# Optimization experiments

Measured on AMD Instinct MI355X. Metric: run time of the kernel, lower is better.

The kernel has to match this reference:

```python
import jax, jax.numpy as jnp
import numpy as np

E, N, H, F = 8, 16384, 1024, 4096  # experts, total tokens, hidden, ffn hidden

def setup_inputs() -> dict:
    key = jax.random.key(0)
    k1, k2, k3 = jax.random.split(key, 3)
    x = jax.random.normal(k1, (N, H), dtype=jnp.float32)
    # original uses torch.rand for weights -> uniform [0,1)
    w1 = jax.random.uniform(k2, (E, H, F), dtype=jnp.float32)
    w2 = jax.random.uniform(k3, (E, F, H), dtype=jnp.float32)
    tokens_per_expert = jnp.full((E,), N // E, dtype=jnp.int32)
    return {
        "permuted_local_hidden_states": x,
        "weight1": w1,
        "weight2": w2,
        "tokens_per_expert": tokens_per_expert,
    }

def reference(permuted_local_hidden_states, weight1, weight2, tokens_per_expert):
    # Grouped GEMM 1: per-expert x[rows_e] @ w1[e]  -> [N, F]
    fc1_output = jax.lax.ragged_dot(permuted_local_hidden_states, weight1, tokens_per_expert)
    # Unfused activation (F.gelu default = exact erf gelu)
    intermediate = jax.nn.gelu(fc1_output, approximate=False)
    # Grouped GEMM 2: per-expert act[rows_e] @ w2[e] -> [N, H]
    fc2_output = jax.lax.ragged_dot(intermediate, weight2, tokens_per_expert)
    return fc2_output
```

## Files before the change

### kernel.cpp

```cpp
#include <hip/hip_runtime.h>
#include <hip/hip_bf16.h>

typedef unsigned short u16;
typedef __attribute__((ext_vector_type(8))) __bf16 bf16x8;
typedef __attribute__((ext_vector_type(4))) float f32x4;
typedef __attribute__((ext_vector_type(4))) float f4v;
typedef __attribute__((ext_vector_type(2))) unsigned short u16x2;
typedef __attribute__((ext_vector_type(4))) unsigned short u16x4;
typedef __attribute__((ext_vector_type(8))) unsigned short u16x8;

__device__ __forceinline__ u16 f32_to_bf16(float f) {
  unsigned int u = __builtin_bit_cast(unsigned int, f);
  u += 0x7FFFu + ((u >> 16) & 1u);
  return (u16)(u >> 16);
}

__device__ __forceinline__ float fast_gelu(float v) {
  float v2 = v * v;
  float t = v * fmaf(0.0713548162726f, v2, 1.5957691216057308f);
  float e = __expf(-t);
  float s = __builtin_amdgcn_rcpf(1.0f + e);
  return v * s;
}

__device__ __forceinline__ void async_ld16(const void* gsrc, void* ldst) {
  __builtin_amdgcn_global_load_lds(
      (__attribute__((address_space(1))) void*)(unsigned long long)gsrc,
      (__attribute__((address_space(3))) void*)(unsigned long long)ldst,
      16, 0, 0);
}

__global__ void cvt_kernel(const float* __restrict__ in, u16* __restrict__ out, int n8) {
  int i = blockIdx.x * blockDim.x + threadIdx.x;
  if (i >= n8) return;
  const f4v* p = (const f4v*)(in + (size_t)i * 8);
  f4v a = p[0], b = p[1];
  u16x8 r;
  r[0] = f32_to_bf16(a[0]); r[1] = f32_to_bf16(a[1]);
  r[2] = f32_to_bf16(a[2]); r[3] = f32_to_bf16(a[3]);
  r[4] = f32_to_bf16(b[0]); r[5] = f32_to_bf16(b[1]);
  r[6] = f32_to_bf16(b[2]); r[7] = f32_to_bf16(b[3]);
  *(u16x8*)(out + (size_t)i * 8) = r;
}

__global__ __launch_bounds__(256)
void tpose_cvt_kernel(const float* __restrict__ in, u16* __restrict__ out, int R, int C) {
  __shared__ u16 tile[64 * 66];
  const int e = blockIdx.z;
  const int c0 = blockIdx.x * 64, r0 = blockIdx.y * 64;
  const float* src = in + (size_t)e * R * C;
  u16* dst = out + (size_t)e * R * C;
  const int t = threadIdx.x;
#pragma unroll
  for (int i = 0; i < 4; ++i) {
    int idx = i * 256 + t;
    int row = idx >> 4, c4 = idx & 15;
    f4v v = *(const f4v*)&src[(size_t)(r0 + row) * C + (c0 + c4 * 4)];
    u16x2 lo, hi;
    lo[0] = f32_to_bf16(v[0]); lo[1] = f32_to_bf16(v[1]);
    hi[0] = f32_to_bf16(v[2]); hi[1] = f32_to_bf16(v[3]);
    *(u16x2*)&tile[row * 66 + c4 * 4] = lo;
    *(u16x2*)&tile[row * 66 + c4 * 4 + 2] = hi;
  }
  __syncthreads();
#pragma unroll
  for (int i = 0; i < 4; ++i) {
    int idx = i * 256 + t;
    int c = idx >> 4, r4 = idx & 15;
    u16x4 v;
#pragma unroll
    for (int j = 0; j < 4; ++j) v[j] = tile[(r4 * 4 + j) * 66 + c];
    *(u16x4*)&dst[(size_t)(c0 + c) * R + r0 + r4 * 4] = v;
  }
}

template <int FUSE>
__global__ __launch_bounds__(512, 2)
void grouped_gemm(const u16* __restrict__ A, const u16* __restrict__ Bt,
                  void* __restrict__ Out, const int* __restrict__ tokens,
                  int Mtot, int K, int Nn) {
  const int NT = Nn >> 8;
  const int id = blockIdx.x;
  const int xcd = id & 7;
  const int within = id >> 3;
  const int slot = xcd + 8 * (within / NT);
  const int ntile = within % NT;

  int row_start = 0, tiles_before = 0;
  int expert = -1, my_row0 = 0, rows_valid = 0;
#pragma unroll
  for (int e = 0; e < 8; ++e) {
    int tk = tokens[e];
    int nt = (tk + 255) >> 8;
    if (expert < 0 && slot >= tiles_before && slot < tiles_before + nt) {
      expert = e;
      int mi = slot - tiles_before;
      my_row0 = row_start + mi * 256;
      rows_valid = tk - mi * 256;
      if (rows_valid > 256) rows_valid = 256;
    }
    tiles_before += nt;
    row_start += tk;
  }
  if (expert < 0) return;

  const int n0 = ntile * 256;
  const u16* Bq = Bt + (size_t)expert * Nn * K + (size_t)n0 * K;

  __shared__ __align__(16) u16 lA[4][8192];
  __shared__ __align__(16) u16 lB[4][8192];

  const int tid = threadIdx.x;
  const int lane = tid & 63;
  const int wave = tid >> 6;
  const int wm = (wave >> 2) * 128;
  const int wn = (wave & 3) * 64;
  const int fr = lane & 15;
  const int fq = lane >> 4;

  f32x4 acc[8][4];
#pragma unroll
  for (int i = 0; i < 8; ++i)
#pragma unroll
    for (int j = 0; j < 4; ++j) acc[i][j] = (f32x4){0.f, 0.f, 0.f, 0.f};

  const int sr = tid >> 2;
  const int swz = ((tid & 3) ^ ((sr >> 1) & 3)) * 8;
  int ga0 = my_row0 + sr;        if (ga0 > Mtot - 1) ga0 = Mtot - 1;
  int ga1 = my_row0 + 128 + sr;  if (ga1 > Mtot - 1) ga1 = Mtot - 1;
  const u16* pA0 = A + (size_t)ga0 * K + swz;
  const u16* pA1 = A + (size_t)ga1 * K + swz;
  const u16* pB0 = Bq + (size_t)sr * K + swz;
  const u16* pB1 = Bq + (size_t)(128 + sr) * K + swz;

  const int cswz = (fq ^ ((fr >> 1) & 3)) * 8;
  const int aoff0 = (wm + fr) * 32 + cswz;
  const int boff0 = (wn + fr) * 32 + cswz;

  const int nslices = K >> 5;

#pragma unroll
  for (int s = 0; s < 3; ++s) {
    async_ld16(pA0 + s * 32, &lA[s][tid * 8]);
    async_ld16(pA1 + s * 32, &lA[s][4096 + tid * 8]);
    async_ld16(pB0 + s * 32, &lB[s][tid * 8]);
    async_ld16(pB1 + s * 32, &lB[s][4096 + tid * 8]);
  }

  bf16x8 aF[4], bF[4];
  for (int sl = 0; sl < nslices; ++sl) {
    const int b = sl & 3;
    const int nb = (sl + 3) & 3;
    const int sk = (sl + 3 < nslices ? sl + 3 : sl) * 32;

    asm volatile("s_waitcnt vmcnt(8)" ::: "memory");
    __builtin_amdgcn_s_barrier();
    asm volatile("" ::: "memory");

    async_ld16(pA0 + sk, &lA[nb][tid * 8]);
    async_ld16(pA1 + sk, &lA[nb][4096 + tid * 8]);
#pragma unroll
    for (int n = 0; n < 4; ++n) bF[n] = *(const bf16x8*)&lB[b][boff0 + n * 512];
#pragma unroll
    for (int m = 0; m < 4; ++m) aF[m] = *(const bf16x8*)&lA[b][aoff0 + m * 512];
    __builtin_amdgcn_s_setprio(1);
#pragma unroll
    for (int m = 0; m < 4; ++m)
#pragma unroll
      for (int n = 0; n < 4; ++n)
        acc[m][n] = __builtin_amdgcn_mfma_f32_16x16x32_bf16(aF[m], bF[n], acc[m][n], 0, 0, 0);
    __builtin_amdgcn_s_setprio(0);
    __builtin_amdgcn_s_barrier();
    asm volatile("" ::: "memory");

    async_ld16(pB0 + sk, &lB[nb][tid * 8]);
    async_ld16(pB1 + sk, &lB[nb][4096 + tid * 8]);
#pragma unroll
    for (int m = 0; m < 4; ++m) aF[m] = *(const bf16x8*)&lA[b][aoff0 + 2048 + m * 512];
    __builtin_amdgcn_s_setprio(1);
#pragma unroll
    for (int m = 0; m < 4; ++m)
#pragma unroll
      for (int n = 0; n < 4; ++n)
        acc[m + 4][n] = __builtin_amdgcn_mfma_f32_16x16x32_bf16(aF[m], bF[n], acc[m + 4][n], 0, 0, 0);
    __builtin_amdgcn_s_setprio(0);
  }

  if (FUSE) {
    u16* Op = (u16*)Out;
#pragma unroll
    for (int m = 0; m < 8; ++m) {
#pragma unroll
      for (int r = 0; r < 4; ++r) {
        int lrow = wm + m * 16 + fq * 4 + r;
        if (lrow < rows_valid) {
          size_t base = (size_t)(my_row0 + lrow) * Nn + (size_t)(n0 + wn + fr);
#pragma unroll
          for (int n = 0; n < 4; ++n)
            Op[base + n * 16] = f32_to_bf16(fast_gelu(acc[m][n][r]));
        }
      }
    }
  } else {
    float* Op = (float*)Out;
#pragma unroll
    for (int m = 0; m < 8; ++m) {
#pragma unroll
      for (int r = 0; r < 4; ++r) {
        int lrow = wm + m * 16 + fq * 4 + r;
        if (lrow < rows_valid) {
          size_t base = (size_t)(my_row0 + lrow) * Nn + (size_t)(n0 + wn + fr);
#pragma unroll
          for (int n = 0; n < 4; ++n) Op[base + n * 16] = acc[m][n][r];
        }
      }
    }
  }
}

extern "C" void kernel_launch(void* const* d_in, const int* in_sizes, int n_in,
                              void* d_out, int out_size, void* d_ws, size_t ws_size,
                              hipStream_t stream) {
  (void)in_sizes; (void)n_in; (void)out_size; (void)ws_size;
  const float* x  = (const float*)d_in[0];
  const float* w1 = (const float*)d_in[1];
  const float* w2 = (const float*)d_in[2];
  const int* tokens = (const int*)d_in[3];

  const int N = 16384, H = 1024, F = 4096, E = 8;

  u16* x_bf  = (u16*)d_ws;
  u16* w1t   = x_bf + (size_t)N * H;
  u16* w2t   = w1t + (size_t)E * F * H;
  u16* inter = w2t + (size_t)E * H * F;

  cvt_kernel<<<dim3((N * H / 8 + 255) / 256), dim3(256), 0, stream>>>(x, x_bf, N * H / 8);
  tpose_cvt_kernel<<<dim3(F / 64, H / 64, E), dim3(256), 0, stream>>>(w1, w1t, H, F);
  tpose_cvt_kernel<<<dim3(H / 64, F / 64, E), dim3(256), 0, stream>>>(w2, w2t, F, H);

  const int SLOTS = N / 256 + E;
  grouped_gemm<1><<<dim3((F / 256) * SLOTS), dim3(512), 0, stream>>>(
      x_bf, w1t, inter, tokens, N, H, F);
  grouped_gemm<0><<<dim3((H / 256) * SLOTS), dim3(512), 0, stream>>>(
      inter, w2t, (float*)d_out, tokens, N, F, H);
}
```

Before: 631.9 us.

## Use narrower N tile for second GEMM and single-barrier pipeline loop

Templates the grouped GEMM on its N tile width and launches the second GEMM with 128-wide tiles, doubling its grid so more CUs stay busy when the output is only 1024 wide. The main loop loads all fragments up front, issues every async load at once and drops the mid-iteration barrier. The transpose tile padding changes from 66 to 65 with scalar LDS writes to cut bank conflicts. Costs are lower B reuse per block in GEMM2, more register pressure from holding all A fragments, and a possible LDS write race now that the second barrier is gone.

```diff
diff --git a/kernel.cpp b/kernel.cpp
--- a/kernel.cpp
+++ b/kernel.cpp
@@ -5,7 +5,6 @@
 typedef __attribute__((ext_vector_type(8))) __bf16 bf16x8;
 typedef __attribute__((ext_vector_type(4))) float f32x4;
 typedef __attribute__((ext_vector_type(4))) float f4v;
-typedef __attribute__((ext_vector_type(2))) unsigned short u16x2;
 typedef __attribute__((ext_vector_type(4))) unsigned short u16x4;
 typedef __attribute__((ext_vector_type(8))) unsigned short u16x8;
 
@@ -45,7 +44,7 @@
 
 __global__ __launch_bounds__(256)
 void tpose_cvt_kernel(const float* __restrict__ in, u16* __restrict__ out, int R, int C) {
-  __shared__ u16 tile[64 * 66];
+  __shared__ u16 tile[64 * 65];
   const int e = blockIdx.z;
   const int c0 = blockIdx.x * 64, r0 = blockIdx.y * 64;
   const float* src = in + (size_t)e * R * C;
@@ -56,11 +55,11 @@
     int idx = i * 256 + t;
     int row = idx >> 4, c4 = idx & 15;
     f4v v = *(const f4v*)&src[(size_t)(r0 + row) * C + (c0 + c4 * 4)];
-    u16x2 lo, hi;
-    lo[0] = f32_to_bf16(v[0]); lo[1] = f32_to_bf16(v[1]);
-    hi[0] = f32_to_bf16(v[2]); hi[1] = f32_to_bf16(v[3]);
-    *(u16x2*)&tile[row * 66 + c4 * 4] = lo;
-    *(u16x2*)&tile[row * 66 + c4 * 4 + 2] = hi;
+    int base = row * 65 + c4 * 4;
+    tile[base + 0] = f32_to_bf16(v[0]);
+    tile[base + 1] = f32_to_bf16(v[1]);
+    tile[base + 2] = f32_to_bf16(v[2]);
+    tile[base + 3] = f32_to_bf16(v[3]);
   }
   __syncthreads();
 #pragma unroll
@@ -69,17 +68,20 @@
     int c = idx >> 4, r4 = idx & 15;
     u16x4 v;
 #pragma unroll
-    for (int j = 0; j < 4; ++j) v[j] = tile[(r4 * 4 + j) * 66 + c];
+    for (int j = 0; j < 4; ++j) v[j] = tile[(r4 * 4 + j) * 65 + c];
     *(u16x4*)&dst[(size_t)(c0 + c) * R + r0 + r4 * 4] = v;
   }
 }
 
-template <int FUSE>
+template <int FUSE, int BN>
 __global__ __launch_bounds__(512, 2)
 void grouped_gemm(const u16* __restrict__ A, const u16* __restrict__ Bt,
                   void* __restrict__ Out, const int* __restrict__ tokens,
                   int Mtot, int K, int Nn) {
-  const int NT = Nn >> 8;
+  constexpr int NF = BN / 64;
+  constexpr int BLOADS = BN / 128;
+  constexpr int LPS = 2 + BLOADS;
+  const int NT = Nn / BN;
   const int id = blockIdx.x;
   const int xcd = id & 7;
   const int within = id >> 3;
@@ -104,25 +106,25 @@
   }
   if (expert < 0) return;
 
-  const int n0 = ntile * 256;
+  const int n0 = ntile * BN;
   const u16* Bq = Bt + (size_t)expert * Nn * K + (size_t)n0 * K;
 
   __shared__ __align__(16) u16 lA[4][8192];
-  __shared__ __align__(16) u16 lB[4][8192];
+  __shared__ __align__(16) u16 lB[4][BN * 32];
 
   const int tid = threadIdx.x;
   const int lane = tid & 63;
   const int wave = tid >> 6;
   const int wm = (wave >> 2) * 128;
-  const int wn = (wave & 3) * 64;
+  const int wn = (wave & 3) * (BN / 4);
   const int fr = lane & 15;
   const int fq = lane >> 4;
 
-  f32x4 acc[8][4];
+  f32x4 acc[8][NF];
 #pragma unroll
   for (int i = 0; i < 8; ++i)
 #pragma unroll
-    for (int j = 0; j < 4; ++j) acc[i][j] = (f32x4){0.f, 0.f, 0.f, 0.f};
+    for (int j = 0; j < NF; ++j) acc[i][j] = (f32x4){0.f, 0.f, 0.f, 0.f};
 
   const int sr = tid >> 2;
   const int swz = ((tid & 3) ^ ((sr >> 1) & 3)) * 8;
@@ -131,7 +133,7 @@
   const u16* pA0 = A + (size_t)ga0 * K + swz;
   const u16* pA1 = A + (size_t)ga1 * K + swz;
   const u16* pB0 = Bq + (size_t)sr * K + swz;
-  const u16* pB1 = Bq + (size_t)(128 + sr) * K + swz;
+  const u16* pB1 = Bq + (size_t)((BN == 256 ? 128 : 0) + sr) * K + swz;
 
   const int cswz = (fq ^ ((fr >> 1) & 3)) * 8;
   const int aoff0 = (wm + fr) * 32 + cswz;
@@ -144,45 +146,43 @@
     async_ld16(pA0 + s * 32, &lA[s][tid * 8]);
     async_ld16(pA1 + s * 32, &lA[s][4096 + tid * 8]);
     async_ld16(pB0 + s * 32, &lB[s][tid * 8]);
-    async_ld16(pB1 + s * 32, &lB[s][4096 + tid * 8]);
-  }
-
-  bf16x8 aF[4], bF[4];
+    if (BLOADS == 2) async_ld16(pB1 + s * 32, &lB[s][4096 + tid * 8]);
+  }
+
   for (int sl = 0; sl < nslices; ++sl) {
     const int b = sl & 3;
     const int nb = (sl + 3) & 3;
     const int sk = (sl + 3 < nslices ? sl + 3 : sl) * 32;
 
-    asm volatile("s_waitcnt vmcnt(8)" ::: "memory");
+    if constexpr (LPS == 4) asm volatile("s_waitcnt vmcnt(8)" ::: "memory");
+    else                    asm volatile("s_waitcnt vmcnt(6)" ::: "memory");
     __builtin_amdgcn_s_barrier();
     asm volatile("" ::: "memory");
 
+    bf16x8 bF[NF], aF0[4], aF1[4];
+#pragma unroll
+    for (int n = 0; n < NF; ++n) bF[n] = *(const bf16x8*)&lB[b][boff0 + n * 512];
+#pragma unroll
+    for (int m = 0; m < 4; ++m) aF0[m] = *(const bf16x8*)&lA[b][aoff0 + m * 512];
+#pragma unroll
+    for (int m = 0; m < 4; ++m) aF1[m] = *(const bf16x8*)&lA[b][aoff0 + 2048 + m * 512];
+
     async_ld16(pA0 + sk, &lA[nb][tid * 8]);
     async_ld16(pA1 + sk, &lA[nb][4096 + tid * 8]);
-#pragma unroll
-    for (int n = 0; n < 4; ++n) bF[n] = *(const bf16x8*)&lB[b][boff0 + n * 512];
-#pragma unroll
-    for (int m = 0; m < 4; ++m) aF[m] = *(const bf16x8*)&lA[b][aoff0 + m * 512];
+    async_ld16(pB0 + sk, &lB[nb][tid * 8]);
+    if (BLOADS == 2) async_ld16(pB1 + sk, &lB[nb][4096 + tid * 8]);
+
     __builtin_amdgcn_s_setprio(1);
 #pragma unroll
     for (int m = 0; m < 4; ++m)
 #pragma unroll
-      for (int n = 0; n < 4; ++n)
-        acc[m][n] = __builtin_amdgcn_mfma_f32_16x16x32_bf16(aF[m], bF[n], acc[m][n], 0, 0, 0);
-    __builtin_amdgcn_s_setprio(0);
-    __builtin_amdgcn_s_barrier();
-    asm volatile("" ::: "memory");
-
-    async_ld16(pB0 + sk, &lB[nb][tid * 8]);
-    async_ld16(pB1 + sk, &lB[nb][4096 + tid * 8]);
-#pragma unroll
-    for (int m = 0; m < 4; ++m) aF[m] = *(const bf16x8*)&lA[b][aoff0 + 2048 + m * 512];
-    __builtin_amdgcn_s_setprio(1);
+      for (int n = 0; n < NF; ++n)
+        acc[m][n] = __builtin_amdgcn_mfma_f32_16x16x32_bf16(aF0[m], bF[n], acc[m][n], 0, 0, 0);
 #pragma unroll
     for (int m = 0; m < 4; ++m)
 #pragma unroll
-      for (int n = 0; n < 4; ++n)
-        acc[m + 4][n] = __builtin_amdgcn_mfma_f32_16x16x32_bf16(aF[m], bF[n], acc[m + 4][n], 0, 0, 0);
+      for (int n = 0; n < NF; ++n)
+        acc[m + 4][n] = __builtin_amdgcn_mfma_f32_16x16x32_bf16(aF1[m], bF[n], acc[m + 4][n], 0, 0, 0);
     __builtin_amdgcn_s_setprio(0);
   }
 
@@ -196,7 +196,7 @@
         if (lrow < rows_valid) {
           size_t base = (size_t)(my_row0 + lrow) * Nn + (size_t)(n0 + wn + fr);
 #pragma unroll
-          for (int n = 0; n < 4; ++n)
+          for (int n = 0; n < NF; ++n)
             Op[base + n * 16] = f32_to_bf16(fast_gelu(acc[m][n][r]));
         }
       }
@@ -211,7 +211,7 @@
         if (lrow < rows_valid) {
           size_t base = (size_t)(my_row0 + lrow) * Nn + (size_t)(n0 + wn + fr);
 #pragma unroll
-          for (int n = 0; n < 4; ++n) Op[base + n * 16] = acc[m][n][r];
+          for (int n = 0; n < NF; ++n) Op[base + n * 16] = acc[m][n][r];
         }
       }
     }
@@ -239,8 +239,8 @@
   tpose_cvt_kernel<<<dim3(H / 64, F / 64, E), dim3(256), 0, stream>>>(w2, w2t, F, H);
 
   const int SLOTS = N / 256 + E;
-  grouped_gemm<1><<<dim3((F / 256) * SLOTS), dim3(512), 0, stream>>>(
+  grouped_gemm<1, 256><<<dim3((F / 256) * SLOTS), dim3(512), 0, stream>>>(
       x_bf, w1t, inter, tokens, N, H, F);
-  grouped_gemm<0><<<dim3((H / 256) * SLOTS), dim3(512), 0, stream>>>(
+  grouped_gemm<0, 128><<<dim3((H / 128) * SLOTS), dim3(512), 0, stream>>>(
       inter, w2t, (float*)d_out, tokens, N, F, H);
 }
```

Result: slower. 670.3 us (+6.1%).

## Reschedule GEMM main-loop barriers and LDS fragment reads around async loads

Applied to the files above, without the earlier changes.

The grouped GEMM inner loop now reads LDS fragments before issuing the next async global-to-LDS loads. It adds explicit lgkmcnt waits and sched_barriers so the MFMA blocks run without interleaved memory ops, uses separate register arrays for the two A halves, and moves the vmcnt wait to the end of each iteration with extra barriers. The goal is to overlap loads with MFMA issue more predictably, at the cost of four workgroup barriers per K-slice instead of two. The weight transpose kernel also changes its LDS padding from 66 to 65 and uses scalar stores, to alter bank-conflict behaviour.

```diff
diff --git a/kernel.cpp b/kernel.cpp
--- a/kernel.cpp
+++ b/kernel.cpp
@@ -5,7 +5,6 @@
 typedef __attribute__((ext_vector_type(8))) __bf16 bf16x8;
 typedef __attribute__((ext_vector_type(4))) float f32x4;
 typedef __attribute__((ext_vector_type(4))) float f4v;
-typedef __attribute__((ext_vector_type(2))) unsigned short u16x2;
 typedef __attribute__((ext_vector_type(4))) unsigned short u16x4;
 typedef __attribute__((ext_vector_type(8))) unsigned short u16x8;
 
@@ -45,7 +44,7 @@
 
 __global__ __launch_bounds__(256)
 void tpose_cvt_kernel(const float* __restrict__ in, u16* __restrict__ out, int R, int C) {
-  __shared__ u16 tile[64 * 66];
+  __shared__ u16 tile[64 * 65];
   const int e = blockIdx.z;
   const int c0 = blockIdx.x * 64, r0 = blockIdx.y * 64;
   const float* src = in + (size_t)e * R * C;
@@ -56,11 +55,11 @@
     int idx = i * 256 + t;
     int row = idx >> 4, c4 = idx & 15;
     f4v v = *(const f4v*)&src[(size_t)(r0 + row) * C + (c0 + c4 * 4)];
-    u16x2 lo, hi;
-    lo[0] = f32_to_bf16(v[0]); lo[1] = f32_to_bf16(v[1]);
-    hi[0] = f32_to_bf16(v[2]); hi[1] = f32_to_bf16(v[3]);
-    *(u16x2*)&tile[row * 66 + c4 * 4] = lo;
-    *(u16x2*)&tile[row * 66 + c4 * 4 + 2] = hi;
+    int base = row * 65 + c4 * 4;
+    tile[base + 0] = f32_to_bf16(v[0]);
+    tile[base + 1] = f32_to_bf16(v[1]);
+    tile[base + 2] = f32_to_bf16(v[2]);
+    tile[base + 3] = f32_to_bf16(v[3]);
   }
   __syncthreads();
 #pragma unroll
@@ -69,7 +68,7 @@
     int c = idx >> 4, r4 = idx & 15;
     u16x4 v;
 #pragma unroll
-    for (int j = 0; j < 4; ++j) v[j] = tile[(r4 * 4 + j) * 66 + c];
+    for (int j = 0; j < 4; ++j) v[j] = tile[(r4 * 4 + j) * 65 + c];
     *(u16x4*)&dst[(size_t)(c0 + c) * R + r0 + r4 * 4] = v;
   }
 }
@@ -146,44 +145,55 @@
     async_ld16(pB0 + s * 32, &lB[s][tid * 8]);
     async_ld16(pB1 + s * 32, &lB[s][4096 + tid * 8]);
   }
-
-  bf16x8 aF[4], bF[4];
+  asm volatile("s_waitcnt vmcnt(8)" ::: "memory");
+  __builtin_amdgcn_s_barrier();
+  asm volatile("" ::: "memory");
+
   for (int sl = 0; sl < nslices; ++sl) {
     const int b = sl & 3;
     const int nb = (sl + 3) & 3;
     const int sk = (sl + 3 < nslices ? sl + 3 : sl) * 32;
 
-    asm volatile("s_waitcnt vmcnt(8)" ::: "memory");
-    __builtin_amdgcn_s_barrier();
-    asm volatile("" ::: "memory");
-
+    bf16x8 bF[4], aF0[4], aF1[4];
+#pragma unroll
+    for (int n = 0; n < 4; ++n) bF[n] = *(const bf16x8*)&lB[b][boff0 + n * 512];
+#pragma unroll
+    for (int m = 0; m < 4; ++m) aF0[m] = *(const bf16x8*)&lA[b][aoff0 + m * 512];
     async_ld16(pA0 + sk, &lA[nb][tid * 8]);
     async_ld16(pA1 + sk, &lA[nb][4096 + tid * 8]);
-#pragma unroll
-    for (int n = 0; n < 4; ++n) bF[n] = *(const bf16x8*)&lB[b][boff0 + n * 512];
-#pragma unroll
-    for (int m = 0; m < 4; ++m) aF[m] = *(const bf16x8*)&lA[b][aoff0 + m * 512];
+    asm volatile("" ::: "memory");
+    __builtin_amdgcn_s_barrier();
+    asm volatile("s_waitcnt lgkmcnt(0)" ::: "memory");
+    __builtin_amdgcn_sched_barrier(0);
     __builtin_amdgcn_s_setprio(1);
 #pragma unroll
     for (int m = 0; m < 4; ++m)
 #pragma unroll
       for (int n = 0; n < 4; ++n)
-        acc[m][n] = __builtin_amdgcn_mfma_f32_16x16x32_bf16(aF[m], bF[n], acc[m][n], 0, 0, 0);
+        acc[m][n] = __builtin_amdgcn_mfma_f32_16x16x32_bf16(aF0[m], bF[n], acc[m][n], 0, 0, 0);
     __builtin_amdgcn_s_setprio(0);
-    __builtin_amdgcn_s_barrier();
-    asm volatile("" ::: "memory");
-
+    asm volatile("" ::: "memory");
+    __builtin_amdgcn_s_barrier();
+    asm volatile("" ::: "memory");
+
+#pragma unroll
+    for (int m = 0; m < 4; ++m) aF1[m] = *(const bf16x8*)&lA[b][aoff0 + 2048 + m * 512];
     async_ld16(pB0 + sk, &lB[nb][tid * 8]);
     async_ld16(pB1 + sk, &lB[nb][4096 + tid * 8]);
-#pragma unroll
-    for (int m = 0; m < 4; ++m) aF[m] = *(const bf16x8*)&lA[b][aoff0 + 2048 + m * 512];
+    asm volatile("s_waitcnt vmcnt(8)" ::: "memory");
+    __builtin_amdgcn_s_barrier();
+    asm volatile("s_waitcnt lgkmcnt(0)" ::: "memory");
+    __builtin_amdgcn_sched_barrier(0);
     __builtin_amdgcn_s_setprio(1);
 #pragma unroll
     for (int m = 0; m < 4; ++m)
 #pragma unroll
       for (int n = 0; n < 4; ++n)
-        acc[m + 4][n] = __builtin_amdgcn_mfma_f32_16x16x32_bf16(aF[m], bF[n], acc[m + 4][n], 0, 0, 0);
+        acc[m + 4][n] = __builtin_amdgcn_mfma_f32_16x16x32_bf16(aF1[m], bF[n], acc[m + 4][n], 0, 0, 0);
     __builtin_amdgcn_s_setprio(0);
+    asm volatile("" ::: "memory");
+    __builtin_amdgcn_s_barrier();
+    asm volatile("" ::: "memory");
   }
 
   if (FUSE) {
```

Result: no change. 642.7 us (+1.7%).

## Shrink GEMM tile to 256x128, triple-buffer, contiguous XCD slot mapping, widen transpose stores

Applied to the files above, without the earlier changes.

The grouped GEMM tile is reduced from 256x256 to 256x128, with each wave now holding a 64x64 accumulator. LDS drops to three buffers so that up to four blocks can fit per CU, and a 3-stage async pipeline with a single barrier per k-slice replaces the 4-stage split-barrier loop. M-tile slots are assigned to XCDs in contiguous ranges balanced across all eight, so idle blocks exit early. The weight transpose kernel now uses a 65-stride tile and 16-byte output stores. Smaller tiles lower arithmetic intensity and raise redundant A reloads, traded for better occupancy and latency hiding.

```diff
diff --git a/kernel.cpp b/kernel.cpp
--- a/kernel.cpp
+++ b/kernel.cpp
@@ -5,8 +5,6 @@
 typedef __attribute__((ext_vector_type(8))) __bf16 bf16x8;
 typedef __attribute__((ext_vector_type(4))) float f32x4;
 typedef __attribute__((ext_vector_type(4))) float f4v;
-typedef __attribute__((ext_vector_type(2))) unsigned short u16x2;
-typedef __attribute__((ext_vector_type(4))) unsigned short u16x4;
 typedef __attribute__((ext_vector_type(8))) unsigned short u16x8;
 
 __device__ __forceinline__ u16 f32_to_bf16(float f) {
@@ -45,7 +43,7 @@
 
 __global__ __launch_bounds__(256)
 void tpose_cvt_kernel(const float* __restrict__ in, u16* __restrict__ out, int R, int C) {
-  __shared__ u16 tile[64 * 66];
+  __shared__ u16 tile[64 * 65];
   const int e = blockIdx.z;
   const int c0 = blockIdx.x * 64, r0 = blockIdx.y * 64;
   const float* src = in + (size_t)e * R * C;
@@ -56,71 +54,77 @@
     int idx = i * 256 + t;
     int row = idx >> 4, c4 = idx & 15;
     f4v v = *(const f4v*)&src[(size_t)(r0 + row) * C + (c0 + c4 * 4)];
-    u16x2 lo, hi;
-    lo[0] = f32_to_bf16(v[0]); lo[1] = f32_to_bf16(v[1]);
-    hi[0] = f32_to_bf16(v[2]); hi[1] = f32_to_bf16(v[3]);
-    *(u16x2*)&tile[row * 66 + c4 * 4] = lo;
-    *(u16x2*)&tile[row * 66 + c4 * 4 + 2] = hi;
+    int base = row * 65 + c4 * 4;
+    tile[base + 0] = f32_to_bf16(v[0]);
+    tile[base + 1] = f32_to_bf16(v[1]);
+    tile[base + 2] = f32_to_bf16(v[2]);
+    tile[base + 3] = f32_to_bf16(v[3]);
   }
   __syncthreads();
 #pragma unroll
-  for (int i = 0; i < 4; ++i) {
+  for (int i = 0; i < 2; ++i) {
     int idx = i * 256 + t;
-    int c = idx >> 4, r4 = idx & 15;
-    u16x4 v;
-#pragma unroll
-    for (int j = 0; j < 4; ++j) v[j] = tile[(r4 * 4 + j) * 66 + c];
-    *(u16x4*)&dst[(size_t)(c0 + c) * R + r0 + r4 * 4] = v;
+    int c = idx >> 3, r8 = idx & 7;
+    u16x8 v;
+#pragma unroll
+    for (int j = 0; j < 8; ++j) v[j] = tile[(r8 * 8 + j) * 65 + c];
+    *(u16x8*)&dst[(size_t)(c0 + c) * R + r0 + r8 * 8] = v;
   }
 }
 
 template <int FUSE>
-__global__ __launch_bounds__(512, 2)
+__global__ __launch_bounds__(512, 4)
 void grouped_gemm(const u16* __restrict__ A, const u16* __restrict__ Bt,
                   void* __restrict__ Out, const int* __restrict__ tokens,
-                  int Mtot, int K, int Nn) {
-  const int NT = Nn >> 8;
+                  int Mtot, int K, int Nn, int ntShift) {
+  const int NT = 1 << ntShift;
   const int id = blockIdx.x;
   const int xcd = id & 7;
   const int within = id >> 3;
-  const int slot = xcd + 8 * (within / NT);
-  const int ntile = within % NT;
+  const int idx = within >> ntShift;
+  const int ntile = within & (NT - 1);
+
+  int nts[8]; int T = 0;
+#pragma unroll
+  for (int e = 0; e < 8; ++e) { nts[e] = (tokens[e] + 255) >> 8; T += nts[e]; }
+  const int q = T >> 3, r = T & 7;
+  const int share = q + (xcd < r ? 1 : 0);
+  if (idx >= share) return;
+  const int slot = xcd * q + (xcd < r ? xcd : r) + idx;
 
   int row_start = 0, tiles_before = 0;
   int expert = -1, my_row0 = 0, rows_valid = 0;
 #pragma unroll
   for (int e = 0; e < 8; ++e) {
-    int tk = tokens[e];
-    int nt = (tk + 255) >> 8;
-    if (expert < 0 && slot >= tiles_before && slot < tiles_before + nt) {
+    int nt = nts[e];
+    if (expert < 0 && slot < tiles_before + nt) {
       expert = e;
       int mi = slot - tiles_before;
       my_row0 = row_start + mi * 256;
-      rows_valid = tk - mi * 256;
+      rows_valid = tokens[e] - mi * 256;
       if (rows_valid > 256) rows_valid = 256;
     }
     tiles_before += nt;
-    row_start += tk;
-  }
-  if (expert < 0) return;
-
-  const int n0 = ntile * 256;
+    row_start += tokens[e];
+  }
+
+  const int n0 = ntile * 128;
   const u16* Bq = Bt + (size_t)expert * Nn * K + (size_t)n0 * K;
 
-  __shared__ __align__(16) u16 lA[4][8192];
-  __shared__ __align__(16) u16 lB[4][8192];
+  __shared__ __align__(16) u16 lA[3][8192];
+  __shared__ __align__(16) u16 lB[3][4096];
 
   const int tid = threadIdx.x;
   const int lane = tid & 63;
   const int wave = tid >> 6;
-  const int wm = (wave >> 2) * 128;
-  const int wn = (wave & 3) * 64;
+  const int wm = (wave >> 1) * 64;
+  const int wn = (wave & 1) * 64;
   const int fr = lane & 15;
   const int fq = lane >> 4;
 
-  f32x4 acc[8][4];
-#pragma unroll
-  for (int i = 0; i < 8; ++i)
+  f32x4 acc[4][4];
+#pragma unroll
+  for (int i = 0; i < 4; ++i)
 #pragma unroll
     for (int j = 0; j < 4; ++j) acc[i][j] = (f32x4){0.f, 0.f, 0.f, 0.f};
 
@@ -130,8 +134,7 @@
   int ga1 = my_row0 + 128 + sr;  if (ga1 > Mtot - 1) ga1 = Mtot - 1;
   const u16* pA0 = A + (size_t)ga0 * K + swz;
   const u16* pA1 = A + (size_t)ga1 * K + swz;
-  const u16* pB0 = Bq + (size_t)sr * K + swz;
-  const u16* pB1 = Bq + (size_t)(128 + sr) * K + swz;
+  const u16* pB  = Bq + (size_t)sr * K + swz;
 
   const int cswz = (fq ^ ((fr >> 1) & 3)) * 8;
   const int aoff0 = (wm + fr) * 32 + cswz;
@@ -139,30 +142,31 @@
 
   const int nslices = K >> 5;
 
-#pragma unroll
-  for (int s = 0; s < 3; ++s) {
-    async_ld16(pA0 + s * 32, &lA[s][tid * 8]);
-    async_ld16(pA1 + s * 32, &lA[s][4096 + tid * 8]);
-    async_ld16(pB0 + s * 32, &lB[s][tid * 8]);
-    async_ld16(pB1 + s * 32, &lB[s][4096 + tid * 8]);
-  }
-
-  bf16x8 aF[4], bF[4];
+  async_ld16(pA0, &lA[0][tid * 8]);
+  async_ld16(pA1, &lA[0][4096 + tid * 8]);
+  async_ld16(pB,  &lB[0][tid * 8]);
+  async_ld16(pA0 + 32, &lA[1][tid * 8]);
+  async_ld16(pA1 + 32, &lA[1][4096 + tid * 8]);
+  async_ld16(pB  + 32, &lB[1][tid * 8]);
+
+  int b = 0, sb = 2;
   for (int sl = 0; sl < nslices; ++sl) {
-    const int b = sl & 3;
-    const int nb = (sl + 3) & 3;
-    const int sk = (sl + 3 < nslices ? sl + 3 : sl) * 32;
-
-    asm volatile("s_waitcnt vmcnt(8)" ::: "memory");
+    const int sk = (sl + 2 < nslices ? sl + 2 : sl) * 32;
+
+    asm volatile("s_waitcnt vmcnt(3)" ::: "memory");
     __builtin_amdgcn_s_barrier();
     asm volatile("" ::: "memory");
 
-    async_ld16(pA0 + sk, &lA[nb][tid * 8]);
-    async_ld16(pA1 + sk, &lA[nb][4096 + tid * 8]);
+    async_ld16(pA0 + sk, &lA[sb][tid * 8]);
+    async_ld16(pA1 + sk, &lA[sb][4096 + tid * 8]);
+    async_ld16(pB  + sk, &lB[sb][tid * 8]);
+
+    bf16x8 aF[4], bF[4];
 #pragma unroll
     for (int n = 0; n < 4; ++n) bF[n] = *(const bf16x8*)&lB[b][boff0 + n * 512];
 #pragma unroll
     for (int m = 0; m < 4; ++m) aF[m] = *(const bf16x8*)&lA[b][aoff0 + m * 512];
+
     __builtin_amdgcn_s_setprio(1);
 #pragma unroll
     for (int m = 0; m < 4; ++m)
@@ -170,48 +174,37 @@
       for (int n = 0; n < 4; ++n)
         acc[m][n] = __builtin_amdgcn_mfma_f32_16x16x32_bf16(aF[m], bF[n], acc[m][n], 0, 0, 0);
     __builtin_amdgcn_s_setprio(0);
-    __builtin_amdgcn_s_barrier();
-    asm volatile("" ::: "memory");
-
-    async_ld16(pB0 + sk, &lB[nb][tid * 8]);
-    async_ld16(pB1 + sk, &lB[nb][4096 + tid * 8]);
-#pragma unroll
-    for (int m = 0; m < 4; ++m) aF[m] = *(const bf16x8*)&lA[b][aoff0 + 2048 + m * 512];
-    __builtin_amdgcn_s_setprio(1);
-#pragma unroll
-    for (int m = 0; m < 4; ++m)
-#pragma unroll
-      for (int n = 0; n < 4; ++n)
-        acc[m + 4][n] = __builtin_amdgcn_mfma_f32_16x16x32_bf16(aF[m], bF[n], acc[m + 4][n], 0, 0, 0);
-    __builtin_amdgcn_s_setprio(0);
+
+    b = (b == 2) ? 0 : b + 1;
+    sb = (sb == 2) ? 0 : sb + 1;
   }
 
   if (FUSE) {
     u16* Op = (u16*)Out;
 #pragma unroll
-    for (int m = 0; m < 8; ++m) {
-#pragma unroll
-      for (int r = 0; r < 4; ++r) {
-        int lrow = wm + m * 16 + fq * 4 + r;
+    for (int m = 0; m < 4; ++m) {
+#pragma unroll
+      for (int r2 = 0; r2 < 4; ++r2) {
+        int lrow = wm + m * 16 + fq * 4 + r2;
         if (lrow < rows_valid) {
           size_t base = (size_t)(my_row0 + lrow) * Nn + (size_t)(n0 + wn + fr);
 #pragma unroll
           for (int n = 0; n < 4; ++n)
-            Op[base + n * 16] = f32_to_bf16(fast_gelu(acc[m][n][r]));
+            Op[base + n * 16] = f32_to_bf16(fast_gelu(acc[m][n][r2]));
         }
       }
     }
   } else {
     float* Op = (float*)Out;
 #pragma unroll
-    for (int m = 0; m < 8; ++m) {
-#pragma unroll
-      for (int r = 0; r < 4; ++r) {
-        int lrow = wm + m * 16 + fq * 4 + r;
+    for (int m = 0; m < 4; ++m) {
+#pragma unroll
+      for (int r2 = 0; r2 < 4; ++r2) {
+        int lrow = wm + m * 16 + fq * 4 + r2;
         if (lrow < rows_valid) {
           size_t base = (size_t)(my_row0 + lrow) * Nn + (size_t)(n0 + wn + fr);
 #pragma unroll
-          for (int n = 0; n < 4; ++n) Op[base + n * 16] = acc[m][n][r];
+          for (int n = 0; n < 4; ++n) Op[base + n * 16] = acc[m][n][r2];
         }
       }
     }
@@ -238,9 +231,8 @@
   tpose_cvt_kernel<<<dim3(F / 64, H / 64, E), dim3(256), 0, stream>>>(w1, w1t, H, F);
   tpose_cvt_kernel<<<dim3(H / 64, F / 64, E), dim3(256), 0, stream>>>(w2, w2t, F, H);
 
-  const int SLOTS = N / 256 + E;
-  grouped_gemm<1><<<dim3((F / 256) * SLOTS), dim3(512), 0, stream>>>(
-      x_bf, w1t, inter, tokens, N, H, F);
-  grouped_gemm<0><<<dim3((H / 256) * SLOTS), dim3(512), 0, stream>>>(
-      inter, w2t, (float*)d_out, tokens, N, F, H);
-}
+  grouped_gemm<1><<<dim3((F / 128) * 72), dim3(512), 0, stream>>>(
+      x_bf, w1t, inter, tokens, N, H, F, 5);
+  grouped_gemm<0><<<dim3((H / 128) * 72), dim3(512), 0, stream>>>(
+      inter, w2t, (float*)d_out, tokens, N, F, H, 3);
+}
```

Measured after the change: 648.8 us. 2.7% more time.
